# Kernel optimization log

Hardware: AMD Instinct MI355X
Metric: run time of the kernel (lower is better)

Reference implementation:

```python
import jax, jax.numpy as jnp
import numpy as np

B, D, H, O, E, K = 8192, 1024, 4096, 1024, 8, 2

def setup_inputs() -> dict:
    key = jax.random.key(0)
    ks = jax.random.split(key, 8)
    x = jax.random.normal(ks[0], (B, D), dtype=jnp.float32)
    topk_idx = jax.random.randint(ks[1], (B, K), 0, E, dtype=jnp.int32)
    weights = jax.random.uniform(ks[2], (B, K), dtype=jnp.float32)
    s1 = 1.0 / np.sqrt(D)
    s2 = 1.0 / np.sqrt(H)
    W1 = jax.random.uniform(ks[3], (E, D, H), minval=-s1, maxval=s1, dtype=jnp.float32)
    b1 = jax.random.uniform(ks[4], (E, H), minval=-s1, maxval=s1, dtype=jnp.float32)
    W2 = jax.random.uniform(ks[5], (E, H, O), minval=-s2, maxval=s2, dtype=jnp.float32)
    b2 = jax.random.uniform(ks[6], (E, O), minval=-s2, maxval=s2, dtype=jnp.float32)
    return {"x": x, "topk_idx": topk_idx, "weights": weights,
            "W1": W1, "b1": b1, "W2": W2, "b2": b2}

def reference(x, topk_idx, weights, W1, b1, W2, b2):
    # Per-token gate mass for each expert: gate[b,e] = sum_i weights[b,i]*[topk_idx[b,i]==e]
    # Equivalent to the original masked gather/scatter combine (duplicates in topk_idx sum).
    out = jnp.zeros((x.shape[0], W2.shape[-1]), dtype=x.dtype)
    for e in range(W1.shape[0]):  # small fixed loop over experts
        gate_e = jnp.sum(weights * (topk_idx == e), axis=1)  # [B]
        h = jax.nn.relu(x @ W1[e] + b1[e])                   # [B,H]
        out_e = h @ W2[e] + b2[e]                            # [B,O]
        out = out + gate_e[:, None] * out_e
    return out
```

## Files before the change

### kernel.cpp

```cpp
#include <hip/hip_runtime.h>
#include <stdint.h>

#define B_TOK 8192
#define D_DIM 1024
#define H_DIM 4096
#define O_DIM 1024
#define E_NUM 8
#define K_TOP 2
#define NPAIR (B_TOK * K_TOP)

typedef short bf16x8 __attribute__((ext_vector_type(8)));
typedef float f32x4 __attribute__((ext_vector_type(4)));

struct Hdr {
    int counts[8];
    int offsets[9];
    int total1, total2;
    int base1[9];
    int base2[9];
};

__device__ __forceinline__ unsigned short f2bf(float f) {
    union { float f; unsigned int u; } v; v.f = f;
    unsigned int u = v.u;
    unsigned int r = (u + 0x7fffu + ((u >> 16) & 1u)) >> 16;
    return (unsigned short)r;
}

__device__ __forceinline__ float bf2f(unsigned short s) {
    union { unsigned int u; float f; } v;
    v.u = ((unsigned int)s) << 16;
    return v.f;
}

__device__ __forceinline__ void async16(const void* g, const void* l) {
    __builtin_amdgcn_global_load_lds(
        (__attribute__((address_space(1))) void*)(uintptr_t)g,
        (__attribute__((address_space(3))) void*)(uint32_t)(uintptr_t)l,
        16, 0, 0);
}

__global__ __launch_bounds__(256) void pre_kernel(
    const float* __restrict__ x, unsigned short* __restrict__ xb,
    const float* __restrict__ W1, const float* __restrict__ W2,
    unsigned short* __restrict__ o1, unsigned short* __restrict__ o2,
    const int* __restrict__ topk, Hdr* __restrict__ hdr,
    int* __restrict__ ptok, int* __restrict__ pslot) {

    __shared__ unsigned short tb[64 * 134];
    int bid = blockIdx.x;
    int tid = threadIdx.x;

    if (bid < 8192) {
        int i = (bid * 256 + tid) * 4;
        float4 v = *(const float4*)(x + i);
        ushort4 o;
        o.x = f2bf(v.x); o.y = f2bf(v.y); o.z = f2bf(v.z); o.w = f2bf(v.w);
        *(ushort4*)(xb + i) = o;
        return;
    }

    if (bid < 16384) {
        int bt = bid - 8192;
        int z = bt >> 9;
        int sub = bt & 511;
        int R, C;
        const float* ip;
        unsigned short* op;
        if (z < 8) {
            R = D_DIM; C = H_DIM;
            ip = W1 + (size_t)z * R * C;
            op = o1 + (size_t)z * R * C;
        } else {
            R = H_DIM; C = O_DIM;
            ip = W2 + (size_t)(z - 8) * R * C;
            op = o2 + (size_t)(z - 8) * R * C;
        }
        int tR = R >> 7;
        int r0 = (sub % tR) * 128;
        int c0 = (sub / tR) * 64;

        int rl = tid >> 4;
        int cg = (tid & 15) * 4;
#pragma unroll
        for (int p = 0; p < 8; p++) {
            int r = rl + p * 16;
            float4 v = *(const float4*)&ip[(size_t)(r0 + r) * C + c0 + cg];
            tb[(cg + 0) * 134 + r] = f2bf(v.x);
            tb[(cg + 1) * 134 + r] = f2bf(v.y);
            tb[(cg + 2) * 134 + r] = f2bf(v.z);
            tb[(cg + 3) * 134 + r] = f2bf(v.w);
        }
        __syncthreads();
        int r16 = (tid & 15) * 8;
#pragma unroll
        for (int i = 0; i < 4; i++) {
            int c = (tid >> 4) + i * 16;
            uint4 v = *(const uint4*)&tb[c * 134 + r16];
            *(uint4*)&op[(size_t)(c0 + c) * R + r0 + r16] = v;
        }
        return;
    }

    int* wcnt = (int*)tb;
    int* wcur = wcnt + 32;
    int w = tid >> 6;
    if ((tid & 63) < 8) wcnt[w * 8 + (tid & 63)] = 0;
    __syncthreads();
    for (int j = 0; j < 64; j++) {
        int e = topk[tid + j * 256];
        atomicAdd(&wcnt[w * 8 + e], 1);
    }
    __syncthreads();
    if (tid == 0) {
        int off = 0, t1 = 0, t2 = 0;
        for (int e = 0; e < 8; e++) {
            int c = 0;
            for (int w2 = 0; w2 < 4; w2++) {
                wcur[w2 * 8 + e] = off + c;
                c += wcnt[w2 * 8 + e];
            }
            hdr->counts[e] = c;
            hdr->offsets[e] = off;
            hdr->base1[e] = t1;
            hdr->base2[e] = t2;
            t1 += ((c + 255) >> 8) * (H_DIM / 256);
            t2 += ((c + 127) >> 7) * (O_DIM / 128);
            off += c;
        }
        hdr->offsets[8] = off;
        hdr->base1[8] = t1;
        hdr->base2[8] = t2;
        hdr->total1 = t1;
        hdr->total2 = t2;
    }
    __syncthreads();
    for (int j = 0; j < 64; j++) {
        int i = tid + j * 256;
        int e = topk[i];
        int pos = atomicAdd(&wcur[w * 8 + e], 1);
        ptok[pos] = i >> 1;
        pslot[i] = pos;
    }
}

__global__ void ws_fail_kernel(float* out) { out[0] = 1.0e9f; }


#define ASL(BUF, KH) ((BUF) * 32768 + (KH) * 16384)

#define STG_A(BUF, KH, KOFF) do { \
    async16(Ab + srcA[0] + (KOFF), smem + ASL(BUF, KH) + wu * 2048); \
    async16(Ab + srcA[1] + (KOFF), smem + ASL(BUF, KH) + wu * 2048 + 1024); } while (0)

#define STG_B(BUF, KH, KOFF) do { \
    async16(Bb + srcB[0] + (KOFF), smem + 65536 + ASL(BUF, KH) + wu * 2048); \
    async16(Bb + srcB[1] + (KOFF), smem + 65536 + ASL(BUF, KH) + wu * 2048 + 1024); } while (0)

#define VM6 asm volatile("s_waitcnt vmcnt(6)" ::: "memory")
#define VM0 asm volatile("s_waitcnt vmcnt(0)" ::: "memory")
#define NOPX ((void)0)

#define PHASE0(BUF, KH, STAGE, CKPT) do { \
    STAGE; \
    bq[0] = *(const bf16x8*)&smem[pBo[0] + ASL(BUF, KH)]; \
    bq[1] = *(const bf16x8*)&smem[pBo[1] + ASL(BUF, KH)]; \
    bq[2] = *(const bf16x8*)&smem[pBo[2] + ASL(BUF, KH)]; \
    bq[3] = *(const bf16x8*)&smem[pBo[3] + ASL(BUF, KH)]; \
    aq[0] = *(const bf16x8*)&smem[pAo[0] + ASL(BUF, KH)]; \
    aq[1] = *(const bf16x8*)&smem[pAo[1] + ASL(BUF, KH)]; \
    aq[2] = *(const bf16x8*)&smem[pAo[2] + ASL(BUF, KH)]; \
    aq[3] = *(const bf16x8*)&smem[pAo[3] + ASL(BUF, KH)]; \
    __builtin_amdgcn_s_barrier(); \
    asm volatile("s_waitcnt lgkmcnt(0)" ::: "memory"); \
    __builtin_amdgcn_s_setprio(1); \
    _Pragma("unroll") \
    for (int q_ = 0; q_ < 4; ++q_) { \
        _Pragma("unroll") \
        for (int n_ = 0; n_ < 4; ++n_) \
            acc[q_][n_] = __builtin_amdgcn_mfma_f32_16x16x32_bf16(aq[q_], bq[n_], acc[q_][n_], 0, 0, 0); \
    } \
    __builtin_amdgcn_s_setprio(0); \
    CKPT; \
    __builtin_amdgcn_s_barrier(); \
} while (0)

#define PHASE1(BUF, KH, STAGE, CKPT) do { \
    STAGE; \
    aq[0] = *(const bf16x8*)&smem[pAo[4] + ASL(BUF, KH)]; \
    aq[1] = *(const bf16x8*)&smem[pAo[5] + ASL(BUF, KH)]; \
    aq[2] = *(const bf16x8*)&smem[pAo[6] + ASL(BUF, KH)]; \
    aq[3] = *(const bf16x8*)&smem[pAo[7] + ASL(BUF, KH)]; \
    __builtin_amdgcn_s_barrier(); \
    asm volatile("s_waitcnt lgkmcnt(0)" ::: "memory"); \
    __builtin_amdgcn_s_setprio(1); \
    _Pragma("unroll") \
    for (int q_ = 0; q_ < 4; ++q_) { \
        _Pragma("unroll") \
        for (int n_ = 0; n_ < 4; ++n_) \
            acc[4 + q_][n_] = __builtin_amdgcn_mfma_f32_16x16x32_bf16(aq[q_], bq[n_], acc[4 + q_][n_], 0, 0, 0); \
    } \
    __builtin_amdgcn_s_setprio(0); \
    CKPT; \
    __builtin_amdgcn_s_barrier(); \
} while (0)

template <int KD, int N, bool GATHER>
__global__ __launch_bounds__(512, 2) void moe_gemm256_kernel(
    const unsigned short* __restrict__ A,
    const unsigned short* __restrict__ Bt,
    const float* __restrict__ bias,
    const Hdr* __restrict__ hdr,
    const int* __restrict__ ptok,
    unsigned short* __restrict__ outp) {

    extern __shared__ __align__(16) char smem[];
    constexpr int NT = KD / 64;
    constexpr int NI = NT / 2;
    static_assert(NT >= 4 && (NT % 2) == 0, "K-tile count");

    const int tid = threadIdx.x;
    const int lane = tid & 63;
    const int wv = tid >> 6;
    const int wu = __builtin_amdgcn_readfirstlane(wv);
    const int lr = lane & 15;
    const int lkg = lane >> 4;
    const int wr = wv >> 2;
    const int wc = wv & 3;

    const int total = hdr->total1;
    const int* tb = hdr->base1;

    int chunk = (total + 7) >> 3;
    int seq = (blockIdx.x & 7) * chunk + (blockIdx.x >> 3);
    if (seq >= total) return;

    int e = 0;
#pragma unroll
    for (int j = 1; j < 8; j++)
        if (seq >= tb[j]) e = j;
    e = __builtin_amdgcn_readfirstlane(e);
    int lt = seq - tb[e];
    int cnt = hdr->counts[e], off = hdr->offsets[e];
    int MT = (cnt + 255) >> 8;
    int mtile = lt % MT, ntile = lt / MT;
    int m0 = mtile * 256, n0 = ntile * 256;

    const char* Ab = (const char*)A;
    const char* Bb = (const char*)(Bt + (size_t)e * ((size_t)N * KD));

    uint32_t srcA[2], srcB[2];
#pragma unroll
    for (int l = 0; l < 2; ++l) {
        int g = wv * 128 + l * 64 + lane;
        int rp = g >> 2, cp = g & 3;
        int c = (cp - (rp >> 1)) & 3;
        int q = off + m0 + rp;
        q = q > NPAIR - 1 ? NPAIR - 1 : q;
        uint32_t rowA = GATHER ? (uint32_t)ptok[q] : (uint32_t)q;
        srcA[l] = rowA * (uint32_t)(KD * 2) + (uint32_t)(c * 16);
        srcB[l] = (uint32_t)(n0 + rp) * (uint32_t)(KD * 2) + (uint32_t)(c * 16);
    }

    uint32_t pAo[8], pBo[4];
#pragma unroll
    for (int mr = 0; mr < 8; ++mr) {
        int r = wr * 128 + mr * 16 + lr;
        pAo[mr] = (uint32_t)(r * 64 + ((lkg + (r >> 1)) & 3) * 16);
    }
#pragma unroll
    for (int nr = 0; nr < 4; ++nr) {
        int r = wc * 64 + nr * 16 + lr;
        pBo[nr] = (uint32_t)(65536 + r * 64 + ((lkg + (r >> 1)) & 3) * 16);
    }

    f32x4 acc[8][4];
#pragma unroll
    for (int i = 0; i < 8; ++i)
#pragma unroll
        for (int j = 0; j < 4; ++j)
            acc[i][j] = (f32x4){0.f, 0.f, 0.f, 0.f};
    bf16x8 aq[4], bq[4];

    STG_A(0, 0, 0u);   STG_B(0, 0, 0u);
    STG_A(0, 1, 64u);  STG_B(0, 1, 64u);
    STG_A(1, 0, 128u); STG_B(1, 0, 128u);
    STG_B(1, 1, 192u);
    VM0;
    __builtin_amdgcn_s_barrier();

    for (int it = 0; it < NI - 1; ++it) {
        const uint32_t kb = (uint32_t)it * 256u;
        PHASE0(0, 0, STG_A(1, 1, kb + 192u), NOPX);
        PHASE1(0, 0, STG_B(0, 0, kb + 256u), NOPX);
        PHASE0(0, 1, STG_A(0, 0, kb + 256u), NOPX);
        PHASE1(0, 1, STG_B(0, 1, kb + 320u), VM6);
        PHASE0(1, 0, STG_A(0, 1, kb + 320u), NOPX);
        PHASE1(1, 0, STG_B(1, 0, kb + 384u), NOPX);
        PHASE0(1, 1, STG_A(1, 0, kb + 384u), NOPX);
        PHASE1(1, 1, STG_B(1, 1, kb + 448u), VM6);
    }
    {
        const uint32_t kb = (uint32_t)(NI - 1) * 256u;
        PHASE0(0, 0, STG_A(1, 1, kb + 192u), NOPX);
        PHASE1(0, 0, NOPX, NOPX);
        PHASE0(0, 1, NOPX, NOPX);
        PHASE1(0, 1, NOPX, VM0);
        PHASE0(1, 0, NOPX, NOPX);
        PHASE1(1, 0, NOPX, NOPX);
        PHASE0(1, 1, NOPX, NOPX);
        PHASE1(1, 1, NOPX, NOPX);
    }

    unsigned short* eb = (unsigned short*)smem;
    int rows_valid = cnt - m0;
    if (rows_valid > 256) rows_valid = 256;
#pragma unroll
    for (int pass = 0; pass < 2; ++pass) {
        __syncthreads();
        if (wr == pass) {
#pragma unroll
            for (int nr = 0; nr < 4; ++nr) {
                int n = wc * 64 + nr * 16 + lr;
                float bv = bias[(size_t)e * N + n0 + n];
#pragma unroll
                for (int mr = 0; mr < 8; ++mr) {
#pragma unroll
                    for (int r2 = 0; r2 < 4; ++r2) {
                        int ml = mr * 16 + lkg * 4 + r2;
                        float v = acc[mr][nr][r2] + bv;
                        if (GATHER) v = v > 0.f ? v : 0.f;
                        eb[ml * 264 + n] = f2bf(v);
                    }
                }
            }
        }
        __syncthreads();
        int rv = rows_valid - pass * 128;
        if (rv > 128) rv = 128;
#pragma unroll
        for (int j = 0; j < 8; ++j) {
            int idx = j * 512 + tid;
            int row = idx >> 5;
            int c16 = idx & 31;
            if (row < rv) {
                uint4 v = *(const uint4*)&eb[row * 264 + c16 * 8];
                *(uint4*)&outp[(size_t)(off + m0 + pass * 128 + row) * N + n0 + c16 * 8] = v;
            }
        }
    }
}

template <int K, int N, bool GATHER>
__global__ __launch_bounds__(256, 4) void moe_gemm128_kernel(
    const unsigned short* __restrict__ A,
    const unsigned short* __restrict__ Bt,
    const float* __restrict__ bias,
    const Hdr* __restrict__ hdr,
    const int* __restrict__ ptok,
    unsigned short* __restrict__ outp) {

    __shared__ __align__(16) unsigned short smem[128 * 132];
    unsigned short* As = smem;
    unsigned short* Bs = smem + 128 * 64;

    const int tid = threadIdx.x;
    const int lane = tid & 63;
    const int wv = tid >> 6;
    const int wu = __builtin_amdgcn_readfirstlane(wv);
    const int wm = (wv & 1) * 64;
    const int wn = (wv >> 1) * 64;
    const int lr = lane & 15;
    const int lkg = lane >> 4;

    const int total = hdr->total2;
    const int* tb = hdr->base2;
    constexpr int NT = N / 128;

    int chunk = (total + 7) >> 3;
    int seq = (blockIdx.x & 7) * chunk + (blockIdx.x >> 3);
    if (seq >= total) return;

    int e = 0;
#pragma unroll
    for (int j = 1; j < 8; j++)
        if (seq >= tb[j]) e = j;
    e = __builtin_amdgcn_readfirstlane(e);
    int lt = seq - tb[e];
    int cnt = hdr->counts[e], off = hdr->offsets[e];
    int MT = (cnt + 127) >> 7;

    int band = lt / (NT * 8);
    int r = lt - band * (NT * 8);
    int mrem = MT - band * 8;
    mrem = mrem > 8 ? 8 : mrem;
    int gsz = mrem * 8;
    int g = r / gsz;
    int rg = r - g * gsz;
    int gm = rg % mrem;
    int gn = rg / mrem;
    int mtile = band * 8 + gm;
    int ntile = g * 8 + gn;
    int m0 = mtile * 128, n0 = ntile * 128;

    const char* Ab = (const char*)A;
    const char* Bb = (const char*)(Bt + (size_t)e * ((size_t)N * K));
    uint32_t offA[4], offB[4];
#pragma unroll
    for (int i = 0; i < 4; i++) {
        int s = i * 256 + tid;
        int rr = s >> 3;
        int cl = (s & 7) ^ (rr & 7);
        int p = off + m0 + rr;
        p = p > NPAIR - 1 ? NPAIR - 1 : p;
        uint32_t row = GATHER ? (uint32_t)ptok[p] : (uint32_t)p;
        offA[i] = (row * (uint32_t)K + (uint32_t)cl * 8u) * 2u;
        offB[i] = (((uint32_t)(n0 + rr)) * (uint32_t)K + (uint32_t)cl * 8u) * 2u;
    }

    f32x4 zero = {0.f, 0.f, 0.f, 0.f};
    f32x4 acc[4][4];
#pragma unroll
    for (int mt = 0; mt < 4; mt++)
#pragma unroll
        for (int nt = 0; nt < 4; nt++) acc[mt][nt] = zero;

    for (int k0 = 0; k0 < K; k0 += 64) {
#pragma unroll
        for (int i = 0; i < 4; i++) {
            async16(Ab + offA[i], &As[(i * 256 + wu * 64) * 8]);
            async16(Bb + offB[i], &Bs[(i * 256 + wu * 64) * 8]);
            offA[i] += 128;
            offB[i] += 128;
        }
        __syncthreads();
#pragma unroll
        for (int ks = 0; ks < 2; ks++) {
            bf16x8 af[4];
#pragma unroll
            for (int q = 0; q < 4; q++) {
                int ra = wm + q * 16 + lr;
                int ca = (ks * 4 + lkg) ^ (ra & 7);
                af[q] = *(const bf16x8*)&As[ra * 64 + ca * 8];
            }
#pragma unroll
            for (int nt = 0; nt < 4; nt++) {
                int rb = wn + nt * 16 + lr;
                int cb = (ks * 4 + lkg) ^ (rb & 7);
                bf16x8 bfr = *(const bf16x8*)&Bs[rb * 64 + cb * 8];
#pragma unroll
                for (int mt = 0; mt < 4; mt++)
                    acc[mt][nt] = __builtin_amdgcn_mfma_f32_16x16x32_bf16(
                        af[mt], bfr, acc[mt][nt], 0, 0, 0);
            }
        }
        __syncthreads();
    }

#pragma unroll
    for (int nt = 0; nt < 4; nt++) {
        int n = wn + nt * 16 + lr;
        float bv = bias[(size_t)e * N + n0 + n];
#pragma unroll
        for (int mt = 0; mt < 4; mt++) {
#pragma unroll
            for (int r2 = 0; r2 < 4; r2++) {
                int m = wm + mt * 16 + lkg * 4 + r2;
                float v = acc[mt][nt][r2] + bv;
                if (GATHER) v = v > 0.f ? v : 0.f;
                smem[m * 132 + n] = f2bf(v);
            }
        }
    }
    __syncthreads();
    int rows_valid = cnt - m0;
    if (rows_valid > 128) rows_valid = 128;
#pragma unroll
    for (int j = 0; j < 16; j++) {
        int idx = j * 256 + tid;
        int row = idx >> 5;
        int lc8 = idx & 31;
        if (row < rows_valid) {
            uint2 v = *(const uint2*)&smem[row * 132 + lc8 * 4];
            *(uint2*)&outp[(size_t)(off + m0 + row) * N + n0 + lc8 * 4] = v;
        }
    }
}

__global__ void combine_kernel(const unsigned short* __restrict__ oslot,
                               const int* __restrict__ pslot,
                               const float* __restrict__ wts,
                               float* __restrict__ out) {
    int tok = blockIdx.x;
    int s0 = pslot[tok * 2], s1 = pslot[tok * 2 + 1];
    float g0 = wts[tok * 2], g1 = wts[tok * 2 + 1];
    int n = threadIdx.x * 4;
    ushort4 a = *(const ushort4*)&oslot[(size_t)s0 * O_DIM + n];
    ushort4 b = *(const ushort4*)&oslot[(size_t)s1 * O_DIM + n];
    float4 o;
    o.x = g0 * bf2f(a.x) + g1 * bf2f(b.x);
    o.y = g0 * bf2f(a.y) + g1 * bf2f(b.y);
    o.z = g0 * bf2f(a.z) + g1 * bf2f(b.z);
    o.w = g0 * bf2f(a.w) + g1 * bf2f(b.w);
    *(float4*)&out[(size_t)tok * O_DIM + n] = o;
}


extern "C" void kernel_launch(void* const* d_in, const int* in_sizes, int n_in,
                              void* d_out, int out_size, void* d_ws, size_t ws_size,
                              hipStream_t stream) {
    const float* x   = (const float*)d_in[0];
    const int* topk  = (const int*)d_in[1];
    const float* wts = (const float*)d_in[2];
    const float* W1  = (const float*)d_in[3];
    const float* b1  = (const float*)d_in[4];
    const float* W2  = (const float*)d_in[5];
    const float* b2  = (const float*)d_in[6];
    float* out = (float*)d_out;

    char* ws = (char*)d_ws;
    size_t off = 0;
    auto alloc = [&](size_t bytes) -> void* {
        void* p = ws + off;
        off += (bytes + 255) & ~(size_t)255;
        return p;
    };
    Hdr* hdr = (Hdr*)alloc(sizeof(Hdr));
    int* ptok = (int*)alloc((size_t)NPAIR * 4);
    int* pslot = (int*)alloc((size_t)NPAIR * 4);
    unsigned short* xb   = (unsigned short*)alloc((size_t)B_TOK * D_DIM * 2);
    unsigned short* W1bt = (unsigned short*)alloc((size_t)E_NUM * D_DIM * H_DIM * 2);
    unsigned short* W2bt = (unsigned short*)alloc((size_t)E_NUM * H_DIM * O_DIM * 2);
    unsigned short* hbuf = (unsigned short*)alloc((size_t)NPAIR * H_DIM * 2);
    unsigned short* oslot = W1bt;

    if (off > ws_size) {
        hipMemsetAsync(d_out, 0, (size_t)out_size * sizeof(float), stream);
        ws_fail_kernel<<<1, 1, 0, stream>>>(out);
        return;
    }

    static int attr_done = 0;
    if (!attr_done) {
        (void)hipFuncSetAttribute(
            reinterpret_cast<const void*>(&moe_gemm256_kernel<D_DIM, H_DIM, true>),
            hipFuncAttributeMaxDynamicSharedMemorySize, 131072);
        attr_done = 1;
    }

    pre_kernel<<<16385, 256, 0, stream>>>(x, xb, W1, W2, W1bt, W2bt,
                                          topk, hdr, ptok, pslot);

    moe_gemm256_kernel<D_DIM, H_DIM, true><<<1152, 512, 131072, stream>>>(
        xb, W1bt, b1, hdr, ptok, hbuf);
    moe_gemm128_kernel<H_DIM, O_DIM, false><<<1152, 256, 0, stream>>>(
        hbuf, W2bt, b2, hdr, ptok, oslot);
    combine_kernel<<<B_TOK, 256, 0, stream>>>(oslot, pslot, wts, out);
}
```

Measured before the change: 722.6 us.

## Fuse gated combine into second expert GEMM via atomic scatter-add

Drops the separate combine kernel and the bf16 per-slot output buffer. The second GEMM now multiplies each row by its gate and atomically adds fp32 results straight into the zeroed output, using token indices and gates staged in shared memory. The routing block moves to block 0 of the prep kernel so it is scheduled early, and GEMM blocks beyond the per-partition chunk exit early. The cost is a memset of the output plus many scattered fp32 atomics per element, which may contend and makes the summation order nondeterministic.

```diff
diff --git a/kernel.cpp b/kernel.cpp
--- a/kernel.cpp
+++ b/kernel.cpp
@@ -44,15 +44,59 @@
     const float* __restrict__ x, unsigned short* __restrict__ xb,
     const float* __restrict__ W1, const float* __restrict__ W2,
     unsigned short* __restrict__ o1, unsigned short* __restrict__ o2,
-    const int* __restrict__ topk, Hdr* __restrict__ hdr,
-    int* __restrict__ ptok, int* __restrict__ pslot) {
+    const int* __restrict__ topk, const float* __restrict__ wts,
+    Hdr* __restrict__ hdr, int* __restrict__ ptok, float* __restrict__ pgate) {
 
     __shared__ unsigned short tb[64 * 134];
     int bid = blockIdx.x;
     int tid = threadIdx.x;
 
-    if (bid < 8192) {
-        int i = (bid * 256 + tid) * 4;
+    if (bid == 0) {
+        int* wcnt = (int*)tb;
+        int* wcur = wcnt + 32;
+        int w = tid >> 6;
+        if ((tid & 63) < 8) wcnt[w * 8 + (tid & 63)] = 0;
+        __syncthreads();
+        for (int j = 0; j < 64; j++) {
+            int e = topk[tid + j * 256];
+            atomicAdd(&wcnt[w * 8 + e], 1);
+        }
+        __syncthreads();
+        if (tid == 0) {
+            int off = 0, t1 = 0, t2 = 0;
+            for (int e = 0; e < 8; e++) {
+                int c = 0;
+                for (int w2 = 0; w2 < 4; w2++) {
+                    wcur[w2 * 8 + e] = off + c;
+                    c += wcnt[w2 * 8 + e];
+                }
+                hdr->counts[e] = c;
+                hdr->offsets[e] = off;
+                hdr->base1[e] = t1;
+                hdr->base2[e] = t2;
+                t1 += ((c + 255) >> 8) * (H_DIM / 256);
+                t2 += ((c + 127) >> 7) * (O_DIM / 128);
+                off += c;
+            }
+            hdr->offsets[8] = off;
+            hdr->base1[8] = t1;
+            hdr->base2[8] = t2;
+            hdr->total1 = t1;
+            hdr->total2 = t2;
+        }
+        __syncthreads();
+        for (int j = 0; j < 64; j++) {
+            int i = tid + j * 256;
+            int e = topk[i];
+            int pos = atomicAdd(&wcur[w * 8 + e], 1);
+            ptok[pos] = i >> 1;
+            pgate[pos] = wts[i];
+        }
+        return;
+    }
+
+    if (bid <= 8192) {
+        int i = ((bid - 1) * 256 + tid) * 4;
         float4 v = *(const float4*)(x + i);
         ushort4 o;
         o.x = f2bf(v.x); o.y = f2bf(v.y); o.z = f2bf(v.z); o.w = f2bf(v.w);
@@ -60,87 +104,43 @@
         return;
     }
 
-    if (bid < 16384) {
-        int bt = bid - 8192;
-        int z = bt >> 9;
-        int sub = bt & 511;
-        int R, C;
-        const float* ip;
-        unsigned short* op;
-        if (z < 8) {
-            R = D_DIM; C = H_DIM;
-            ip = W1 + (size_t)z * R * C;
-            op = o1 + (size_t)z * R * C;
-        } else {
-            R = H_DIM; C = O_DIM;
-            ip = W2 + (size_t)(z - 8) * R * C;
-            op = o2 + (size_t)(z - 8) * R * C;
-        }
-        int tR = R >> 7;
-        int r0 = (sub % tR) * 128;
-        int c0 = (sub / tR) * 64;
-
-        int rl = tid >> 4;
-        int cg = (tid & 15) * 4;
-#pragma unroll
-        for (int p = 0; p < 8; p++) {
-            int r = rl + p * 16;
-            float4 v = *(const float4*)&ip[(size_t)(r0 + r) * C + c0 + cg];
-            tb[(cg + 0) * 134 + r] = f2bf(v.x);
-            tb[(cg + 1) * 134 + r] = f2bf(v.y);
-            tb[(cg + 2) * 134 + r] = f2bf(v.z);
-            tb[(cg + 3) * 134 + r] = f2bf(v.w);
-        }
-        __syncthreads();
-        int r16 = (tid & 15) * 8;
-#pragma unroll
-        for (int i = 0; i < 4; i++) {
-            int c = (tid >> 4) + i * 16;
-            uint4 v = *(const uint4*)&tb[c * 134 + r16];
-            *(uint4*)&op[(size_t)(c0 + c) * R + r0 + r16] = v;
-        }
-        return;
-    }
-
-    int* wcnt = (int*)tb;
-    int* wcur = wcnt + 32;
-    int w = tid >> 6;
-    if ((tid & 63) < 8) wcnt[w * 8 + (tid & 63)] = 0;
+    int bt = bid - 8193;
+    int z = bt >> 9;
+    int sub = bt & 511;
+    int R, C;
+    const float* ip;
+    unsigned short* op;
+    if (z < 8) {
+        R = D_DIM; C = H_DIM;
+        ip = W1 + (size_t)z * R * C;
+        op = o1 + (size_t)z * R * C;
+    } else {
+        R = H_DIM; C = O_DIM;
+        ip = W2 + (size_t)(z - 8) * R * C;
+        op = o2 + (size_t)(z - 8) * R * C;
+    }
+    int tR = R >> 7;
+    int r0 = (sub % tR) * 128;
+    int c0 = (sub / tR) * 64;
+
+    int rl = tid >> 4;
+    int cg = (tid & 15) * 4;
+#pragma unroll
+    for (int p = 0; p < 8; p++) {
+        int r = rl + p * 16;
+        float4 v = *(const float4*)&ip[(size_t)(r0 + r) * C + c0 + cg];
+        tb[(cg + 0) * 134 + r] = f2bf(v.x);
+        tb[(cg + 1) * 134 + r] = f2bf(v.y);
+        tb[(cg + 2) * 134 + r] = f2bf(v.z);
+        tb[(cg + 3) * 134 + r] = f2bf(v.w);
+    }
     __syncthreads();
-    for (int j = 0; j < 64; j++) {
-        int e = topk[tid + j * 256];
-        atomicAdd(&wcnt[w * 8 + e], 1);
-    }
-    __syncthreads();
-    if (tid == 0) {
-        int off = 0, t1 = 0, t2 = 0;
-        for (int e = 0; e < 8; e++) {
-            int c = 0;
-            for (int w2 = 0; w2 < 4; w2++) {
-                wcur[w2 * 8 + e] = off + c;
-                c += wcnt[w2 * 8 + e];
-            }
-            hdr->counts[e] = c;
-            hdr->offsets[e] = off;
-            hdr->base1[e] = t1;
-            hdr->base2[e] = t2;
-            t1 += ((c + 255) >> 8) * (H_DIM / 256);
-            t2 += ((c + 127) >> 7) * (O_DIM / 128);
-            off += c;
-        }
-        hdr->offsets[8] = off;
-        hdr->base1[8] = t1;
-        hdr->base2[8] = t2;
-        hdr->total1 = t1;
-        hdr->total2 = t2;
-    }
-    __syncthreads();
-    for (int j = 0; j < 64; j++) {
-        int i = tid + j * 256;
-        int e = topk[i];
-        int pos = atomicAdd(&wcur[w * 8 + e], 1);
-        ptok[pos] = i >> 1;
-        pslot[i] = pos;
+    int r16 = (tid & 15) * 8;
+#pragma unroll
+    for (int i = 0; i < 4; i++) {
+        int c = (tid >> 4) + i * 16;
+        uint4 v = *(const uint4*)&tb[c * 134 + r16];
+        *(uint4*)&op[(size_t)(c0 + c) * R + r0 + r16] = v;
     }
 }
 
@@ -232,7 +232,9 @@
     const int* tb = hdr->base1;
 
     int chunk = (total + 7) >> 3;
-    int seq = (blockIdx.x & 7) * chunk + (blockIdx.x >> 3);
+    int idx = blockIdx.x >> 3;
+    if (idx >= chunk) return;
+    int seq = (blockIdx.x & 7) * chunk + idx;
     if (seq >= total) return;
 
     int e = 0;
@@ -340,9 +342,9 @@
         if (rv > 128) rv = 128;
 #pragma unroll
         for (int j = 0; j < 8; ++j) {
-            int idx = j * 512 + tid;
-            int row = idx >> 5;
-            int c16 = idx & 31;
+            int idx2 = j * 512 + tid;
+            int row = idx2 >> 5;
+            int c16 = idx2 & 31;
             if (row < rv) {
                 uint4 v = *(const uint4*)&eb[row * 264 + c16 * 8];
                 *(uint4*)&outp[(size_t)(off + m0 + pass * 128 + row) * N + n0 + c16 * 8] = v;
@@ -351,14 +353,15 @@
     }
 }
 
-template <int K, int N, bool GATHER>
+template <int K, int N>
 __global__ __launch_bounds__(256, 4) void moe_gemm128_kernel(
     const unsigned short* __restrict__ A,
     const unsigned short* __restrict__ Bt,
     const float* __restrict__ bias,
     const Hdr* __restrict__ hdr,
     const int* __restrict__ ptok,
-    unsigned short* __restrict__ outp) {
+    const float* __restrict__ pgate,
+    float* __restrict__ out) {
 
     __shared__ __align__(16) unsigned short smem[128 * 132];
     unsigned short* As = smem;
@@ -378,7 +381,9 @@
     constexpr int NT = N / 128;
 
     int chunk = (total + 7) >> 3;
-    int seq = (blockIdx.x & 7) * chunk + (blockIdx.x >> 3);
+    int idx = blockIdx.x >> 3;
+    if (idx >= chunk) return;
+    int seq = (blockIdx.x & 7) * chunk + idx;
     if (seq >= total) return;
 
     int e = 0;
@@ -413,8 +418,7 @@
         int cl = (s & 7) ^ (rr & 7);
         int p = off + m0 + rr;
         p = p > NPAIR - 1 ? NPAIR - 1 : p;
-        uint32_t row = GATHER ? (uint32_t)ptok[p] : (uint32_t)p;
-        offA[i] = (row * (uint32_t)K + (uint32_t)cl * 8u) * 2u;
+        offA[i] = ((uint32_t)p * (uint32_t)K + (uint32_t)cl * 8u) * 2u;
         offB[i] = (((uint32_t)(n0 + rr)) * (uint32_t)K + (uint32_t)cl * 8u) * 2u;
     }
 
@@ -457,6 +461,17 @@
         __syncthreads();
     }
 
+    int rows_valid = cnt - m0;
+    if (rows_valid > 128) rows_valid = 128;
+    int* tokl = (int*)smem;
+    float* gatel = (float*)((char*)smem + 512);
+    if (tid < 128) {
+        bool v = tid < rows_valid;
+        int slot = off + m0 + tid;
+        tokl[tid] = v ? ptok[slot] : -1;
+        gatel[tid] = v ? pgate[slot] : 0.f;
+    }
+    __syncthreads();
 #pragma unroll
     for (int nt = 0; nt < 4; nt++) {
         int n = wn + nt * 16 + lr;
@@ -466,43 +481,13 @@
 #pragma unroll
             for (int r2 = 0; r2 < 4; r2++) {
                 int m = wm + mt * 16 + lkg * 4 + r2;
-                float v = acc[mt][nt][r2] + bv;
-                if (GATHER) v = v > 0.f ? v : 0.f;
-                smem[m * 132 + n] = f2bf(v);
+                int t = tokl[m];
+                if (t >= 0)
+                    atomicAdd(&out[(size_t)t * N + n0 + n],
+                              gatel[m] * (acc[mt][nt][r2] + bv));
             }
         }
     }
-    __syncthreads();
-    int rows_valid = cnt - m0;
-    if (rows_valid > 128) rows_valid = 128;
-#pragma unroll
-    for (int j = 0; j < 16; j++) {
-        int idx = j * 256 + tid;
-        int row = idx >> 5;
-        int lc8 = idx & 31;
-        if (row < rows_valid) {
-            uint2 v = *(const uint2*)&smem[row * 132 + lc8 * 4];
-            *(uint2*)&outp[(size_t)(off + m0 + row) * N + n0 + lc8 * 4] = v;
-        }
-    }
-}
-
-__global__ void combine_kernel(const unsigned short* __restrict__ oslot,
-                               const int* __restrict__ pslot,
-                               const float* __restrict__ wts,
-                               float* __restrict__ out) {
-    int tok = blockIdx.x;
-    int s0 = pslot[tok * 2], s1 = pslot[tok * 2 + 1];
-    float g0 = wts[tok * 2], g1 = wts[tok * 2 + 1];
-    int n = threadIdx.x * 4;
-    ushort4 a = *(const ushort4*)&oslot[(size_t)s0 * O_DIM + n];
-    ushort4 b = *(const ushort4*)&oslot[(size_t)s1 * O_DIM + n];
-    float4 o;
-    o.x = g0 * bf2f(a.x) + g1 * bf2f(b.x);
-    o.y = g0 * bf2f(a.y) + g1 * bf2f(b.y);
-    o.z = g0 * bf2f(a.z) + g1 * bf2f(b.z);
-    o.w = g0 * bf2f(a.w) + g1 * bf2f(b.w);
-    *(float4*)&out[(size_t)tok * O_DIM + n] = o;
 }
 
 
@@ -527,12 +512,11 @@
     };
     Hdr* hdr = (Hdr*)alloc(sizeof(Hdr));
     int* ptok = (int*)alloc((size_t)NPAIR * 4);
-    int* pslot = (int*)alloc((size_t)NPAIR * 4);
+    float* pgate = (float*)alloc((size_t)NPAIR * 4);
     unsigned short* xb   = (unsigned short*)alloc((size_t)B_TOK * D_DIM * 2);
     unsigned short* W1bt = (unsigned short*)alloc((size_t)E_NUM * D_DIM * H_DIM * 2);
     unsigned short* W2bt = (unsigned short*)alloc((size_t)E_NUM * H_DIM * O_DIM * 2);
     unsigned short* hbuf = (unsigned short*)alloc((size_t)NPAIR * H_DIM * 2);
-    unsigned short* oslot = W1bt;
 
     if (off > ws_size) {
         hipMemsetAsync(d_out, 0, (size_t)out_size * sizeof(float), stream);
@@ -548,12 +532,13 @@
         attr_done = 1;
     }
 
+    hipMemsetAsync(out, 0, (size_t)B_TOK * O_DIM * sizeof(float), stream);
+
     pre_kernel<<<16385, 256, 0, stream>>>(x, xb, W1, W2, W1bt, W2bt,
-                                          topk, hdr, ptok, pslot);
+                                          topk, wts, hdr, ptok, pgate);
 
     moe_gemm256_kernel<D_DIM, H_DIM, true><<<1152, 512, 131072, stream>>>(
         xb, W1bt, b1, hdr, ptok, hbuf);
-    moe_gemm128_kernel<H_DIM, O_DIM, false><<<1152, 256, 0, stream>>>(
-        hbuf, W2bt, b2, hdr, ptok, oslot);
-    combine_kernel<<<B_TOK, 256, 0, stream>>>(oslot, pslot, wts, out);
-}
+    moe_gemm128_kernel<H_DIM, O_DIM><<<1152, 256, 0, stream>>>(
+        hbuf, W2bt, b2, hdr, ptok, pgate, out);
+}
```

Measured after the change: 771.8 us. +6.8%, slower.
